# Kernel tuning notes

Hardware: AMD Instinct MI355X
Metric: run time of the kernel (lower is better)

## Reference

```python
import jax, jax.numpy as jnp
import numpy as np

B, S, D = 2, 4096, 768
H, DH = 12, 64
BLK = 64
NB = S // BLK
L, F = 2, 3072
V, POS = 50358, 4096
NS, NL = 8, 2
NKV = 8  # 3 sliding-window + 2 global + 3 random key blocks per query block
SCALE = 1.0 / np.sqrt(DH)


def layer_norm(x, g, b):
    m = jnp.mean(x, -1, keepdims=True)
    v = jnp.mean(jnp.square(x - m), -1, keepdims=True)
    return (x - m) * jax.lax.rsqrt(v + 1e-12) * g + b


def block_sparse_attention(x, mask, w_qkv, b_qkv, rand_blocks):
    # x: [B,S,D], w_qkv: [3,D,D], rand_blocks: [NB,3] int block ids
    qkv = jnp.einsum('bsd,tde->tbse', x, w_qkv) + b_qkv[:, None, None, :]
    q, k, v = [a.reshape(B, S, H, DH).transpose(0, 2, 1, 3) for a in qkv]  # [B,H,S,DH]
    qb = q.reshape(B, H, NB, BLK, DH)
    kb = k.reshape(B, H, NB, BLK, DH)
    vb = v.reshape(B, H, NB, BLK, DH)
    ar = jnp.arange(NB)
    win = jnp.clip(ar[:, None] + jnp.arange(-1, 2)[None, :], 0, NB - 1)  # [NB,3]
    glb = jnp.broadcast_to(jnp.array([0, NB - 1]), (NB, 2))              # [NB,2]
    idx = jnp.concatenate([win, glb, rand_blocks], axis=1)               # [NB,NKV]
    kg = kb[:, :, idx].reshape(B, H, NB, NKV * BLK, DH)                  # gathered keys
    vg = vb[:, :, idx].reshape(B, H, NB, NKV * BLK, DH)
    mg = mask.reshape(B, NB, BLK)[:, idx].reshape(B, NB, NKV * BLK)
    scores = jnp.einsum('bhnqd,bhnkd->bhnqk', qb, kg) * SCALE
    scores = scores + (mg[:, None, :, None, :] - 1.0) * 1e9
    out = jnp.einsum('bhnqk,bhnkd->bhnqd', jax.nn.softmax(scores, -1), vg)  # [B,H,NB,BLK,DH]
    # global query blocks (first/last) attend densely to the full sequence
    qg = jnp.concatenate([qb[:, :, 0], qb[:, :, NB - 1]], axis=2)  # [B,H,2*BLK,DH]
    sg = jnp.einsum('bhqd,bhkd->bhqk', qg, k) * SCALE + (mask[:, None, None, :] - 1.0) * 1e9
    og = jnp.einsum('bhqk,bhkd->bhqd', jax.nn.softmax(sg, -1), v)
    out = out.at[:, :, 0].set(og[:, :, :BLK]).at[:, :, NB - 1].set(og[:, :, BLK:])
    return out.reshape(B, H, S, DH).transpose(0, 2, 1, 3).reshape(B, S, D)


def setup_inputs() -> dict:
    key = jax.random.key(0)
    ks = iter(jax.random.split(key, 40))
    p = lambda shape: (0.02 * jax.random.normal(next(ks), shape)).astype(jnp.float32)
    inp = {}
    inp['input_ids'] = jax.random.randint(next(ks), (B, S), 0, V, dtype=jnp.int32)
    inp['attention_mask'] = jnp.ones((B, S), jnp.float32)
    inp['token_type_ids'] = jnp.zeros((B, S), jnp.int32)
    st = jax.random.randint(next(ks), (B, NS), 0, S - 65, dtype=jnp.int32)
    ln_ = jax.random.randint(next(ks), (B, NS), 1, 65, dtype=jnp.int32)
    inp['spans'] = jnp.stack([st, st + ln_], axis=-1)  # [B,NS,2], start < end
    inp['rand_blocks'] = jax.random.randint(next(ks), (NB, 3), 0, NB, dtype=jnp.int32)
    inp['word_emb'] = p((V, D))
    inp['pos_emb'] = p((POS, D))
    inp['type_emb'] = p((2, D))
    inp['emb_ln_g'] = jnp.ones((D,), jnp.float32)
    inp['emb_ln_b'] = jnp.zeros((D,), jnp.float32)
    inp['qkv_w'] = p((L, 3, D, D))
    inp['qkv_b'] = jnp.zeros((L, 3, D), jnp.float32)
    inp['attn_out_w'] = p((L, D, D))
    inp['attn_out_b'] = jnp.zeros((L, D), jnp.float32)
    inp['ln1_g'] = jnp.ones((L, D), jnp.float32)
    inp['ln1_b'] = jnp.zeros((L, D), jnp.float32)
    inp['ff1_w'] = p((L, D, F))
    inp['ff1_b'] = jnp.zeros((L, F), jnp.float32)
    inp['ff2_w'] = p((L, F, D))
    inp['ff2_b'] = jnp.zeros((L, D), jnp.float32)
    inp['ln2_g'] = jnp.ones((L, D), jnp.float32)
    inp['ln2_b'] = jnp.zeros((L, D), jnp.float32)
    inp['head_w'] = p((D, NL))
    inp['head_b'] = jnp.zeros((NL,), jnp.float32)
    return inp


def reference(input_ids, attention_mask, token_type_ids, spans, rand_blocks,
              word_emb, pos_emb, type_emb, emb_ln_g, emb_ln_b,
              qkv_w, qkv_b, attn_out_w, attn_out_b, ln1_g, ln1_b,
              ff1_w, ff1_b, ff2_w, ff2_b, ln2_g, ln2_b, head_w, head_b):
    h = word_emb[input_ids] + pos_emb[None, :S] + type_emb[token_type_ids]
    h = layer_norm(h, emb_ln_g, emb_ln_b)
    for l in range(L):
        a = block_sparse_attention(h, attention_mask, qkv_w[l], qkv_b[l], rand_blocks)
        h = layer_norm(h + a @ attn_out_w[l] + attn_out_b[l], ln1_g[l], ln1_b[l])
        ff = jax.nn.gelu(h @ ff1_w[l] + ff1_b[l]) @ ff2_w[l] + ff2_b[l]
        h = layer_norm(h + ff, ln2_g[l], ln2_b[l])
    # span mean pooling: mean of h[b, s:e] for each (s,e) span
    starts, ends = spans[..., 0], spans[..., 1]
    pos = jnp.arange(S)
    span_mask = ((pos >= starts[..., None]) & (pos < ends[..., None])).astype(h.dtype)  # [B,NS,S]
    ent = jnp.einsum('bns,bsd->bnd', span_mask, h) / (ends - starts)[..., None].astype(h.dtype)
    pred = ent @ head_w + head_b  # [B,NS,NL]
    return pred.reshape(B * NS, NL)
```

## Files before the change

### kernel.cpp

```cpp
#include <hip/hip_runtime.h>

constexpr int B = 2, S = 4096, D = 768, H = 12, DH = 64, BLK = 64, NB = 64, NKV = 8;
constexpr int F = 3072, NS = 8, M = B * S;
constexpr int NCH = 8;
constexpr float SCALE = 0.125f;
constexpr float L2E = 1.44269504088896f;
constexpr long HD = (long)M * D;

using u16 = unsigned short;
using u32 = unsigned int;
using bf16 = __bf16;
using bf16x8 = __attribute__((ext_vector_type(8))) bf16;
using f32x4 = __attribute__((ext_vector_type(4))) float;

constexpr long DD = (long)D * D;
constexpr long DF = (long)D * F;
constexpr long OFF_AO  = 6 * DD;
constexpr long OFF_FF1 = 8 * DD;
constexpr long OFF_FF2 = 8 * DD + 2 * DF;

__device__ __forceinline__ u16 f2bf(float x) {
  u32 u = __builtin_bit_cast(u32, x);
  u = (u + 0x7fffu + ((u >> 16) & 1u)) >> 16;
  return (u16)u;
}
__device__ __forceinline__ u32 pack2(float a, float b) {
  return (u32)f2bf(a) | ((u32)f2bf(b) << 16);
}
__device__ __forceinline__ float bf2f(u16 v) {
  return __builtin_bit_cast(float, (u32)v << 16);
}
__device__ __forceinline__ float fast_gelu(float x) {
  float u = 0.7978845608028654f * (x + 0.044715f * x * x * x);
  float t = __expf(u + u);
  return x - x * __builtin_amdgcn_rcpf(t + 1.f);
}

__device__ __forceinline__ void gload16(const void* g, void* l) {
  __builtin_amdgcn_global_load_lds(
      (const __attribute__((address_space(1))) u32*)g,
      (__attribute__((address_space(3))) u32*)l, 16, 0, 0);
}

__global__ __launch_bounds__(256) void wtrans_kern(
    const float* __restrict__ in, u16* __restrict__ out, int K, int N, long inz, long outz)
{
  in += (long)blockIdx.z * inz; out += (long)blockIdx.z * outz;
  __shared__ float T[32][33];
  const int n0 = blockIdx.x * 32, k0 = blockIdx.y * 32;
  const int c = threadIdx.x & 31, r8 = threadIdx.x >> 5;
  #pragma unroll
  for (int i = 0; i < 4; ++i)
    T[r8 + i * 8][c] = in[(long)(k0 + r8 + i * 8) * N + n0 + c];
  __syncthreads();
  #pragma unroll
  for (int i = 0; i < 4; ++i)
    out[(long)(n0 + r8 + i * 8) * K + k0 + c] = f2bf(T[c][r8 + i * 8]);
}

__global__ __launch_bounds__(256) void embed_ln_kern(
    const int* __restrict__ ids, const int* __restrict__ tt,
    const float* __restrict__ we, const float* __restrict__ pe, const float* __restrict__ te,
    const float* __restrict__ g, const float* __restrict__ bb,
    u16* __restrict__ h)
{
  const long i = (long)blockIdx.x * 4 + (threadIdx.x >> 6);
  const int lane = threadIdx.x & 63;
  const int c = lane * 4;
  const int s = (int)(i & (S - 1));
  const long wo = (long)ids[i] * D;
  const long to = (long)tt[i] * D;
  const long po = (long)s * D;
  float4 x0, x1, x2;
  {
    float4 a0 = *(const float4*)(we + wo + c),       p0 = *(const float4*)(pe + po + c),
           t0 = *(const float4*)(te + to + c);
    float4 a1 = *(const float4*)(we + wo + c + 256), p1 = *(const float4*)(pe + po + c + 256),
           t1 = *(const float4*)(te + to + c + 256);
    float4 a2 = *(const float4*)(we + wo + c + 512), p2 = *(const float4*)(pe + po + c + 512),
           t2 = *(const float4*)(te + to + c + 512);
    x0 = make_float4(a0.x+p0.x+t0.x, a0.y+p0.y+t0.y, a0.z+p0.z+t0.z, a0.w+p0.w+t0.w);
    x1 = make_float4(a1.x+p1.x+t1.x, a1.y+p1.y+t1.y, a1.z+p1.z+t1.z, a1.w+p1.w+t1.w);
    x2 = make_float4(a2.x+p2.x+t2.x, a2.y+p2.y+t2.y, a2.z+p2.z+t2.z, a2.w+p2.w+t2.w);
  }
  float sm = x0.x+x0.y+x0.z+x0.w + x1.x+x1.y+x1.z+x1.w + x2.x+x2.y+x2.z+x2.w;
  float sq = x0.x*x0.x+x0.y*x0.y+x0.z*x0.z+x0.w*x0.w
           + x1.x*x1.x+x1.y*x1.y+x1.z*x1.z+x1.w*x1.w
           + x2.x*x2.x+x2.y*x2.y+x2.z*x2.z+x2.w*x2.w;
  #pragma unroll
  for (int o = 32; o; o >>= 1) { sm += __shfl_xor(sm, o); sq += __shfl_xor(sq, o); }
  const float mean = sm * (1.f / D);
  const float var  = sq * (1.f / D) - mean * mean;
  const float rs   = rsqrtf(var + 1e-12f);
  float4 g0 = *(const float4*)(g + c),  g1 = *(const float4*)(g + c + 256),
         g2 = *(const float4*)(g + c + 512);
  float4 b0 = *(const float4*)(bb + c), b1 = *(const float4*)(bb + c + 256),
         b2 = *(const float4*)(bb + c + 512);
  u16* rb = h + i * D;
  *(uint2*)(rb + c)       = make_uint2(pack2((x0.x-mean)*rs*g0.x+b0.x, (x0.y-mean)*rs*g0.y+b0.y),
                                       pack2((x0.z-mean)*rs*g0.z+b0.z, (x0.w-mean)*rs*g0.w+b0.w));
  *(uint2*)(rb + c + 256) = make_uint2(pack2((x1.x-mean)*rs*g1.x+b1.x, (x1.y-mean)*rs*g1.y+b1.y),
                                       pack2((x1.z-mean)*rs*g1.z+b1.z, (x1.w-mean)*rs*g1.w+b1.w));
  *(uint2*)(rb + c + 512) = make_uint2(pack2((x2.x-mean)*rs*g2.x+b2.x, (x2.y-mean)*rs*g2.y+b2.y),
                                       pack2((x2.z-mean)*rs*g2.z+b2.z, (x2.w-mean)*rs*g2.w+b2.w));
}

__global__ __launch_bounds__(256) void ln_kern(
    u16* __restrict__ h, const float* __restrict__ g, const float* __restrict__ bb)
{
  const long i = (long)blockIdx.x * 4 + (threadIdx.x >> 6);
  const int lane = threadIdx.x & 63;
  const int c = lane * 4;
  u16* row = h + i * D;
  uint2 u0 = *(const uint2*)(row + c);
  uint2 u1 = *(const uint2*)(row + c + 256);
  uint2 u2 = *(const uint2*)(row + c + 512);
  float x[12];
  x[0] = bf2f(u0.x); x[1] = bf2f(u0.x >> 16); x[2] = bf2f(u0.y); x[3] = bf2f(u0.y >> 16);
  x[4] = bf2f(u1.x); x[5] = bf2f(u1.x >> 16); x[6] = bf2f(u1.y); x[7] = bf2f(u1.y >> 16);
  x[8] = bf2f(u2.x); x[9] = bf2f(u2.x >> 16); x[10] = bf2f(u2.y); x[11] = bf2f(u2.y >> 16);
  float sm = 0.f, sq = 0.f;
  #pragma unroll
  for (int j = 0; j < 12; ++j) { sm += x[j]; sq += x[j] * x[j]; }
  #pragma unroll
  for (int o = 32; o; o >>= 1) { sm += __shfl_xor(sm, o); sq += __shfl_xor(sq, o); }
  const float mean = sm * (1.f / D);
  const float var  = sq * (1.f / D) - mean * mean;
  const float rs   = rsqrtf(var + 1e-12f);
  float4 g0 = *(const float4*)(g + c),  g1 = *(const float4*)(g + c + 256),
         g2 = *(const float4*)(g + c + 512);
  float4 b0 = *(const float4*)(bb + c), b1 = *(const float4*)(bb + c + 256),
         b2 = *(const float4*)(bb + c + 512);
  *(uint2*)(row + c)       = make_uint2(pack2((x[0]-mean)*rs*g0.x+b0.x, (x[1]-mean)*rs*g0.y+b0.y),
                                        pack2((x[2]-mean)*rs*g0.z+b0.z, (x[3]-mean)*rs*g0.w+b0.w));
  *(uint2*)(row + c + 256) = make_uint2(pack2((x[4]-mean)*rs*g1.x+b1.x, (x[5]-mean)*rs*g1.y+b1.y),
                                        pack2((x[6]-mean)*rs*g1.z+b1.z, (x[7]-mean)*rs*g1.w+b1.w));
  *(uint2*)(row + c + 512) = make_uint2(pack2((x[8]-mean)*rs*g2.x+b2.x, (x[9]-mean)*rs*g2.y+b2.y),
                                        pack2((x[10]-mean)*rs*g2.z+b2.z, (x[11]-mean)*rs*g2.w+b2.w));
}

__global__ __launch_bounds__(256) void mgemm_kern(
    const u16* __restrict__ A, const u16* __restrict__ Wt,
    const float* __restrict__ bias, void* __restrict__ Cv,
    int N, int K, long wz, long bz, long cz, int mode, int ksplit)
{
  const int z = blockIdx.z;
  int k0 = 0, kend = K;
  if (ksplit > 1) {
    const int kch = K / ksplit;
    k0 = z * kch; kend = k0 + kch;
  } else {
    Wt += (long)z * wz; bias += (long)z * bz;
  }
  const int gx = gridDim.x;
  const int nwg = gx * gridDim.y;
  int bid = blockIdx.y * gx + blockIdx.x;
  bid = (bid & 7) * (nwg >> 3) + (bid >> 3);
  const long bm = (long)(bid / gx) * 128;
  const int bn = (bid % gx) * 128;

  const int tid = threadIdx.x;
  const int lane = tid & 63, w = tid >> 6;
  const int wm = w >> 1, wn = w & 1;
  const int ls = lane >> 4, lr = lane & 15;

  __shared__ u16 LB[32768];
  u16* const St0 = LB;
  u16* const St1 = LB + 16384;
  float* const LBf = (float*)LB;

  f32x4 acc[4][4];
  #pragma unroll
  for (int i = 0; i < 4; ++i)
    #pragma unroll
    for (int j = 0; j < 4; ++j)
      acc[i][j] = (f32x4){0.f, 0.f, 0.f, 0.f};

  auto STAGE = [&](u16* buf, int kk) {
    #pragma unroll
    for (int c = 0; c < 4; ++c) {
      const int n = (w * 4 + c) * 64 + lane;
      const int row = n >> 3;
      const int kc2 = (n & 7) ^ (row & 7);
      gload16(A  + (bm + row) * K + kk + kc2 * 8, buf + (w * 4 + c) * 512);
      gload16(Wt + (long)(bn + row) * K + kk + kc2 * 8, buf + 8192 + (w * 4 + c) * 512);
    }
  };

  STAGE(St0, k0);
  int cur = 0;
  for (int kk = k0; kk < kend; kk += 64) {
    if (kk + 64 < kend) {
      STAGE(cur ? St0 : St1, kk + 64);
      asm volatile("s_waitcnt vmcnt(8)" ::: "memory");
    } else {
      asm volatile("s_waitcnt vmcnt(0)" ::: "memory");
    }
    __builtin_amdgcn_s_barrier();
    __builtin_amdgcn_sched_barrier(0);
    const u16* AsL = cur ? St1 : St0;
    const u16* BsL = AsL + 8192;
    __builtin_amdgcn_s_setprio(1);
    #pragma unroll
    for (int ks = 0; ks < 2; ++ks) {
      bf16x8 af[4], bv[4];
      const int kc = ks * 4 + ls;
      const int sw = (kc ^ (lr & 7)) << 3;
      #pragma unroll
      for (int mf = 0; mf < 4; ++mf)
        af[mf] = *(const bf16x8*)&AsL[(wm * 64 + mf * 16 + lr) * 64 + sw];
      #pragma unroll
      for (int nf = 0; nf < 4; ++nf)
        bv[nf] = *(const bf16x8*)&BsL[(wn * 64 + nf * 16 + lr) * 64 + sw];
      #pragma unroll
      for (int mf = 0; mf < 4; ++mf)
        #pragma unroll
        for (int nf = 0; nf < 4; ++nf)
          acc[mf][nf] = __builtin_amdgcn_mfma_f32_16x16x32_bf16(
              af[mf], bv[nf], acc[mf][nf], 0, 0, 0);
    }
    __builtin_amdgcn_s_setprio(0);
    __builtin_amdgcn_s_barrier();
    cur ^= 1;
  }

  u16* Cu = (u16*)Cv + (long)z * cz;
  const int r0 = ls * 4;

  if (mode == 2) {
    #pragma unroll
    for (int nf = 0; nf < 4; ++nf) {
      const int col = wn * 64 + nf * 16 + lr;
      const float bvv = bias[bn + col];
      #pragma unroll
      for (int mf = 0; mf < 4; ++mf) {
        #pragma unroll
        for (int r = 0; r < 4; ++r) {
          const int rowl = wm * 64 + mf * 16 + r0 + r;
          LBf[rowl * 128 + (col ^ ((rowl & 7) << 3))] = acc[mf][nf][r] + bvv;
        }
      }
    }
    __syncthreads();
    const int c0 = (tid & 15) * 8;
    #pragma unroll
    for (int i = 0; i < 8; ++i) {
      const int gr = (tid >> 4) + i * 16;
      const int cs = c0 ^ ((gr & 7) << 3);
      float4 a4 = *(const float4*)&LBf[gr * 128 + cs];
      float4 b4 = *(const float4*)&LBf[gr * 128 + cs + 4];
      u16* dst = Cu + (bm + gr) * N + bn + c0;
      uint4 res = *(const uint4*)dst;
      uint4 out;
      out.x = pack2(a4.x + bf2f(res.x), a4.y + bf2f(res.x >> 16));
      out.y = pack2(a4.z + bf2f(res.y), a4.w + bf2f(res.y >> 16));
      out.z = pack2(b4.x + bf2f(res.z), b4.y + bf2f(res.z >> 16));
      out.w = pack2(b4.z + bf2f(res.w), b4.w + bf2f(res.w >> 16));
      *(uint4*)dst = out;
    }
    return;
  }

  if (mode == 1 || (mode == 4 && bn < 1536)) {
    const int t = (mode == 4) ? (bn / 768) : 0;
    const int cl0 = (mode == 4) ? (bn - t * 768) : bn;
    const int Nt = (mode == 4) ? 768 : N;
    u16* Cd = (mode == 4) ? (Cu + (long)t * HD) : Cu;
    #pragma unroll
    for (int nf = 0; nf < 4; ++nf) {
      const int col = wn * 64 + nf * 16 + lr;
      const float bvv = bias[bn + col];
      #pragma unroll
      for (int mf = 0; mf < 4; ++mf) {
        #pragma unroll
        for (int r = 0; r < 4; ++r) {
          const int rowl = wm * 64 + mf * 16 + r0 + r;
          float vv = acc[mf][nf][r] + bvv;
          if (mode == 1) vv = fast_gelu(vv);
          LB[rowl * 128 + (col ^ ((rowl & 7) << 3))] = f2bf(vv);
        }
      }
    }
    __syncthreads();
    const int c0 = (tid & 15) * 8;
    #pragma unroll
    for (int i = 0; i < 8; ++i) {
      const int gr = (tid >> 4) + i * 16;
      uint4 v4 = *(const uint4*)&LB[gr * 128 + (c0 ^ ((gr & 7) << 3))];
      *(uint4*)(Cd + (bm + gr) * Nt + cl0 + c0) = v4;
    }
    return;
  }

  #pragma unroll
  for (int nf = 0; nf < 4; ++nf) {
    const int cl = bn - 1536 + wn * 64 + nf * 16 + lr;
    const int hcol = cl >> 6, dcol = cl & 63;
    const float bvv = bias[1536 + cl];
    #pragma unroll
    for (int mf = 0; mf < 4; ++mf) {
      const long t0 = bm + wm * 64 + mf * 16 + r0;
      const int bb2 = (int)(t0 >> 12), s0 = (int)(t0 & (S - 1));
      const float v0 = acc[mf][nf][0] + bvv, v1 = acc[mf][nf][1] + bvv;
      const float v2 = acc[mf][nf][2] + bvv, v3 = acc[mf][nf][3] + bvv;
      *(uint2*)(Cu + 2 * HD + (((long)bb2 * H + hcol) * 64 + dcol) * S + s0) =
          make_uint2(pack2(v0, v1), pack2(v2, v3));
    }
  }
}

__global__ __launch_bounds__(256) void mattn_kern(
    const u16* __restrict__ q, const u16* __restrict__ k, const u16* __restrict__ vt,
    const float* __restrict__ mask, const int* __restrict__ rb,
    u16* __restrict__ ctx, float* __restrict__ part)
{
  int lin = blockIdx.x;
  lin = (lin & 7) * 234 + (lin >> 3);
  const int x  = lin % 78;
  const int hh = (lin / 78) % H;
  const int b  = lin / 936;

  int qb, kv0, nkv, qb2 = 0, ch = 0, dense;
  if (x < 62) { dense = 0; qb = x + 1; kv0 = 0; nkv = NKV; }
  else {
    dense = 1;
    const int dx = x - 62;
    qb2 = dx >> 3; ch = dx & 7;
    qb = qb2 ? NB - 1 : 0; kv0 = ch * (NB / NCH); nkv = NB / NCH;
  }
  const int tid = threadIdx.x, lane = tid & 63, w = tid >> 6;
  const int lr = lane & 15, hi = lane >> 4;

  __shared__ u16 KV[2][8192];
  __shared__ u16 Ps[64][72];

  const long qrow0 = (long)b * S + qb * 64;
  bf16x8 qf[2];
  {
    const u16* qp = q + (qrow0 + w * 16 + lr) * D + hh * 64 + hi * 8;
    qf[0] = *(const bf16x8*)(qp);
    qf[1] = *(const bf16x8*)(qp + 32);
  }
  const long vtbase = (((long)b * H + hh) * 64) * S;

  bf16x8 ones8;
  #pragma unroll
  for (int i = 0; i < 8; ++i) ones8[i] = __builtin_bit_cast(bf16, (u16)0x3F80);

  auto kbof = [&](int j) -> int {
    if (dense) return kv0 + j;
    if (j < 3) return qb - 1 + j;
    if (j == 3) return 0;
    if (j == 4) return NB - 1;
    return rb[qb * 3 + (j - 5)];
  };

  auto STAGE = [&](u16* st, int kb) {
    const long krow0 = (long)b * S + kb * 64;
    #pragma unroll
    for (int c = 0; c < 2; ++c) {
      const int n = (w * 2 + c) * 64 + lane;
      const int row = n >> 3;
      const int g2 = (n & 7) ^ (row & 7);
      gload16(k + (krow0 + row) * D + hh * 64 + g2 * 8, st + (w * 2 + c) * 512);
      gload16(vt + vtbase + (long)row * S + kb * 64 + g2 * 8, st + 4096 + (w * 2 + c) * 512);
    }
  };

  f32x4 acc[4];
  #pragma unroll
  for (int nf = 0; nf < 4; ++nf) acc[nf] = (f32x4){0.f, 0.f, 0.f, 0.f};
  f32x4 lacc = (f32x4){0.f, 0.f, 0.f, 0.f};
  float m_run = -1e30f;

  const float C2 = SCALE * L2E;

  float4 mk4[4];
  auto LOADMASK = [&](int kb) {
    const long r = (long)b * S + kb * 64;
    #pragma unroll
    for (int kf = 0; kf < 4; ++kf)
      mk4[kf] = *(const float4*)(mask + r + kf * 16 + hi * 4);
  };

  STAGE(KV[0], kbof(0));
  LOADMASK(kbof(0));

  for (int jj = 0; jj < nkv; ++jj) {
    if (jj + 1 < nkv) {
      STAGE(KV[(jj + 1) & 1], kbof(jj + 1));
      asm volatile("s_waitcnt vmcnt(4)" ::: "memory");
    } else {
      asm volatile("s_waitcnt vmcnt(0)" ::: "memory");
    }
    __builtin_amdgcn_s_barrier();
    __builtin_amdgcn_sched_barrier(0);

    const u16* Ks = KV[jj & 1];
    const u16* Vs = Ks + 4096;

    f32x4 sc[4];
    #pragma unroll
    for (int kf = 0; kf < 4; ++kf) sc[kf] = (f32x4){0.f, 0.f, 0.f, 0.f};
    __builtin_amdgcn_s_setprio(1);
    #pragma unroll
    for (int kc = 0; kc < 2; ++kc) {
      #pragma unroll
      for (int kf = 0; kf < 4; ++kf) {
        const int g2 = ((kc * 4 + hi) ^ (lr & 7)) << 3;
        bf16x8 kfr = *(const bf16x8*)&Ks[(kf * 16 + lr) * 64 + g2];
        sc[kf] = __builtin_amdgcn_mfma_f32_16x16x32_bf16(kfr, qf[kc], sc[kf], 0, 0, 0);
      }
    }
    __builtin_amdgcn_s_setprio(0);

    float sv[4][4];
    float mx = -3.0e38f;
    #pragma unroll
    for (int kf = 0; kf < 4; ++kf) {
      const float mka[4] = {mk4[kf].x, mk4[kf].y, mk4[kf].z, mk4[kf].w};
      #pragma unroll
      for (int r = 0; r < 4; ++r) {
        sv[kf][r] = sc[kf][r] * C2 + (mka[r] - 1.f) * (1e9f * L2E);
        mx = fmaxf(mx, sv[kf][r]);
      }
    }
    mx = fmaxf(mx, __shfl_xor(mx, 16));
    mx = fmaxf(mx, __shfl_xor(mx, 32));
    const bool need = mx > m_run + 8.f;
    if (__any((int)need)) {
      const float mn = fmaxf(m_run, mx);
      const float al = exp2f(m_run - mn);
      m_run = mn;
      #pragma unroll
      for (int r = 0; r < 4; ++r) {
        const float alr = __shfl(al, (lane & 48) | (hi * 4 + r));
        lacc[r] *= alr;
        acc[0][r] *= alr; acc[1][r] *= alr; acc[2][r] *= alr; acc[3][r] *= alr;
      }
    }
    {
      const int prow = w * 16 + lr;
      #pragma unroll
      for (int kf = 0; kf < 4; ++kf) {
        u32 lo = pack2(exp2f(sv[kf][0] - m_run), exp2f(sv[kf][1] - m_run));
        u32 hi2 = pack2(exp2f(sv[kf][2] - m_run), exp2f(sv[kf][3] - m_run));
        *(uint2*)&Ps[prow][kf * 16 + hi * 4] = make_uint2(lo, hi2);
      }
    }

    __builtin_amdgcn_s_setprio(1);
    #pragma unroll
    for (int kc = 0; kc < 2; ++kc) {
      bf16x8 pf = *(const bf16x8*)&Ps[w * 16 + lr][kc * 32 + hi * 8];
      #pragma unroll
      for (int nf = 0; nf < 4; ++nf) {
        const int g2 = ((kc * 4 + hi) ^ (lr & 7)) << 3;
        bf16x8 vfr = *(const bf16x8*)&Vs[(nf * 16 + lr) * 64 + g2];
        acc[nf] = __builtin_amdgcn_mfma_f32_16x16x32_bf16(pf, vfr, acc[nf], 0, 0, 0);
      }
      lacc = __builtin_amdgcn_mfma_f32_16x16x32_bf16(pf, ones8, lacc, 0, 0, 0);
    }
    __builtin_amdgcn_s_setprio(0);

    if (jj + 1 < nkv) LOADMASK(kbof(jj + 1));

    __builtin_amdgcn_s_barrier();
  }

  if (!dense) {
    #pragma unroll
    for (int r = 0; r < 4; ++r) {
      const float inv = 1.f / lacc[r];
      const int prow = w * 16 + hi * 4 + r;
      Ps[prow][ 0 + lr] = f2bf(acc[0][r] * inv);
      Ps[prow][16 + lr] = f2bf(acc[1][r] * inv);
      Ps[prow][32 + lr] = f2bf(acc[2][r] * inv);
      Ps[prow][48 + lr] = f2bf(acc[3][r] * inv);
    }
    __syncthreads();
    const int r2 = tid >> 2, c2 = (tid & 3) * 16;
    uint4 v0 = *(const uint4*)&Ps[r2][c2];
    uint4 v1 = *(const uint4*)&Ps[r2][c2 + 8];
    u16* op = ctx + (qrow0 + r2) * D + hh * 64 + c2;
    *(uint4*)(op)     = v0;
    *(uint4*)(op + 8) = v1;
  } else {
    const long pb = ((((long)b * H + hh) * 2 + qb2) * NCH + ch) * (64 * 68);
    #pragma unroll
    for (int r = 0; r < 4; ++r) {
      const float m_r = __shfl(m_run, (lane & 48) | (hi * 4 + r));
      float* pp = part + pb + (w * 16 + hi * 4 + r) * 68;
      pp[ 0 + lr] = acc[0][r];
      pp[16 + lr] = acc[1][r];
      pp[32 + lr] = acc[2][r];
      pp[48 + lr] = acc[3][r];
      if (lr == 0) { pp[64] = m_r; pp[65] = lacc[r]; }
    }
  }
}

__global__ __launch_bounds__(256) void attn_combine_kern(
    const float* __restrict__ part, u16* __restrict__ ctx)
{
  const int g = blockIdx.x;
  const int qb2 = g & 1;
  const int hh = (g >> 1) % H;
  const int b  = g / (2 * H);
  const int r  = threadIdx.x >> 2;
  const int d0 = (threadIdx.x & 3) * 16;
  const long pb = (long)g * NCH * 64 * 68;
  float mg = -1e30f;
  for (int ch = 0; ch < NCH; ++ch)
    mg = fmaxf(mg, part[pb + ch * 64 * 68 + r * 68 + 64]);
  float lg = 0.f;
  float a[16] = {};
  for (int ch = 0; ch < NCH; ++ch) {
    const float* pp = part + pb + ch * 64 * 68 + r * 68;
    const float w = exp2f(pp[64] - mg);
    lg += pp[65] * w;
    #pragma unroll
    for (int i = 0; i < 4; ++i) {
      float4 t4 = *(const float4*)(pp + d0 + i * 4);
      a[i*4+0] += t4.x * w; a[i*4+1] += t4.y * w; a[i*4+2] += t4.z * w; a[i*4+3] += t4.w * w;
    }
  }
  const int qb = qb2 ? NB - 1 : 0;
  const float inv = 1.f / lg;
  u16* op = ctx + ((long)b * S + qb * 64 + r) * D + hh * 64 + d0;
  #pragma unroll
  for (int i = 0; i < 4; ++i)
    *(uint2*)(op + i * 4) = make_uint2(pack2(a[i*4+0]*inv, a[i*4+1]*inv),
                                       pack2(a[i*4+2]*inv, a[i*4+3]*inv));
}

__global__ __launch_bounds__(256) void span_head_kern(
    const u16* __restrict__ h, const int* __restrict__ spans,
    const float* __restrict__ hw, const float* __restrict__ hb, float* __restrict__ out)
{
  __shared__ float s0[4], s1[4];
  const int bn = blockIdx.x;
  const int tid = threadIdx.x;
  const int st = spans[bn * 2], en = spans[bn * 2 + 1];
  const int b = bn >> 3;
  float a0 = 0.f, a1 = 0.f, a2 = 0.f;
  for (int s = st; s < en; ++s) {
    const u16* row = h + ((long)b * S + s) * D;
    a0 += bf2f(row[tid]); a1 += bf2f(row[tid + 256]); a2 += bf2f(row[tid + 512]);
  }
  const float inv = 1.f / (float)(en - st);
  a0 *= inv; a1 *= inv; a2 *= inv;
  float p0 = a0 * hw[tid * 2]     + a1 * hw[(tid + 256) * 2]     + a2 * hw[(tid + 512) * 2];
  float p1 = a0 * hw[tid * 2 + 1] + a1 * hw[(tid + 256) * 2 + 1] + a2 * hw[(tid + 512) * 2 + 1];
  #pragma unroll
  for (int o = 32; o; o >>= 1) { p0 += __shfl_xor(p0, o); p1 += __shfl_xor(p1, o); }
  if ((tid & 63) == 0) { s0[tid >> 6] = p0; s1[tid >> 6] = p1; }
  __syncthreads();
  if (tid == 0) {
    out[bn * 2]     = s0[0] + s0[1] + s0[2] + s0[3] + hb[0];
    out[bn * 2 + 1] = s1[0] + s1[1] + s1[2] + s1[3] + hb[1];
  }
}

extern "C" void kernel_launch(void* const* d_in, const int* in_sizes, int n_in,
                              void* d_out, int out_size, void* d_ws, size_t ws_size,
                              hipStream_t stream) {
  const int*   input_ids  = (const int*)  d_in[0];
  const float* attn_mask  = (const float*)d_in[1];
  const int*   tok_type   = (const int*)  d_in[2];
  const int*   spans      = (const int*)  d_in[3];
  const int*   rand_blk   = (const int*)  d_in[4];
  const float* word_emb   = (const float*)d_in[5];
  const float* pos_emb    = (const float*)d_in[6];
  const float* type_emb   = (const float*)d_in[7];
  const float* emb_g      = (const float*)d_in[8];
  const float* emb_b      = (const float*)d_in[9];
  const float* qkv_w      = (const float*)d_in[10];
  const float* qkv_b      = (const float*)d_in[11];
  const float* aow        = (const float*)d_in[12];
  const float* aob        = (const float*)d_in[13];
  const float* ln1g       = (const float*)d_in[14];
  const float* ln1b       = (const float*)d_in[15];
  const float* ff1w       = (const float*)d_in[16];
  const float* ff1b       = (const float*)d_in[17];
  const float* ff2w       = (const float*)d_in[18];
  const float* ff2b       = (const float*)d_in[19];
  const float* ln2g       = (const float*)d_in[20];
  const float* ln2b       = (const float*)d_in[21];
  const float* headw      = (const float*)d_in[22];
  const float* headb      = (const float*)d_in[23];

  float* ws    = (float*)d_ws;
  u16*   h     = (u16*)ws;
  u16*   qkvb  = (u16*)(ws + HD);
  u16*   ffb   = (u16*)(ws + HD);
  u16*   ctx16 = (u16*)(ws + 3 * HD);
  float* part  = ws + 4 * HD;
  u16*   wb    = (u16*)(ws + 4 * HD + HD/2);

  wtrans_kern<<<dim3(24, 24, 6), dim3(256), 0, stream>>>(qkv_w, wb, D, D, DD, DD);
  wtrans_kern<<<dim3(24, 24, 2), dim3(256), 0, stream>>>(aow, wb + OFF_AO, D, D, DD, DD);
  wtrans_kern<<<dim3(96, 24, 2), dim3(256), 0, stream>>>(ff1w, wb + OFF_FF1, D, F, DF, DF);
  wtrans_kern<<<dim3(24, 96, 2), dim3(256), 0, stream>>>(ff2w, wb + OFF_FF2, F, D, DF, DF);

  embed_ln_kern<<<dim3(M / 4), dim3(256), 0, stream>>>(
      input_ids, tok_type, word_emb, pos_emb, type_emb, emb_g, emb_b, h);

  for (int l = 0; l < 2; ++l) {
    mgemm_kern<<<dim3(18, 64, 1), dim3(256), 0, stream>>>(
        h, wb + (long)l * 3 * DD, qkv_b + (long)l * 3 * D, qkvb, 2304, D, 0, 0, 0, 4, 1);
    mattn_kern<<<dim3(1872), dim3(256), 0, stream>>>(
        qkvb, qkvb + HD, qkvb + 2 * HD, attn_mask, rand_blk, ctx16, part);
    attn_combine_kern<<<dim3(B * H * 2), dim3(256), 0, stream>>>(part, ctx16);
    mgemm_kern<<<dim3(6, 64, 1), dim3(256), 0, stream>>>(
        ctx16, wb + OFF_AO + (long)l * DD, aob + (long)l * D, h, D, D, 0, 0, 0, 2, 1);
    ln_kern<<<dim3(M / 4), dim3(256), 0, stream>>>(h, ln1g + (long)l * D, ln1b + (long)l * D);
    mgemm_kern<<<dim3(24, 64, 1), dim3(256), 0, stream>>>(
        h, wb + OFF_FF1 + (long)l * DF, ff1b + (long)l * F, ffb, F, D, 0, 0, 0, 1, 1);
    mgemm_kern<<<dim3(6, 64, 1), dim3(256), 0, stream>>>(
        ffb, wb + OFF_FF2 + (long)l * DF, ff2b + (long)l * D, h, D, F, 0, 0, 0, 2, 1);
    ln_kern<<<dim3(M / 4), dim3(256), 0, stream>>>(h, ln2g + (long)l * D, ln2b + (long)l * D);
  }

  span_head_kern<<<dim3(B * NS), dim3(256), 0, stream>>>(h, spans, headw, headb, (float*)d_out);
}
```

Before: 547.2 us.

## Single-buffer A tile in GEMM to cut LDS footprint and raise occupancy

Only the weight (B) tile stays double-buffered. The activation (A) tile becomes a single LDS buffer that is reloaded after the compute barrier, which shrinks shared memory from 64KB to 48KB per workgroup. The mode-2 residual epilogue now stages the fp32 output in two 64-row halves so it fits in the smaller buffer. The aim is more resident workgroups per CU. The cost is that A loads are no longer overlapped with compute, since they are issued only after the barrier and waited on before the next iteration.

Result: slower. 586.3 us (+7.1%).

```diff
diff --git a/kernel.cpp b/kernel.cpp
--- a/kernel.cpp
+++ b/kernel.cpp
@@ -164,10 +164,10 @@
   const int wm = w >> 1, wn = w & 1;
   const int ls = lane >> 4, lr = lane & 15;
 
-  __shared__ u16 LB[32768];
-  u16* const St0 = LB;
-  u16* const St1 = LB + 16384;
-  float* const LBf = (float*)LB;
+  __shared__ u16 LB[24576];
+  u16* const As = LB;
+  u16* const B0 = LB + 8192;
+  u16* const B1 = LB + 16384;
 
   f32x4 acc[4][4];
   #pragma unroll
@@ -176,30 +176,39 @@
     for (int j = 0; j < 4; ++j)
       acc[i][j] = (f32x4){0.f, 0.f, 0.f, 0.f};
 
-  auto STAGE = [&](u16* buf, int kk) {
+  auto STAGE_A = [&](int kk) {
     #pragma unroll
     for (int c = 0; c < 4; ++c) {
       const int n = (w * 4 + c) * 64 + lane;
       const int row = n >> 3;
       const int kc2 = (n & 7) ^ (row & 7);
-      gload16(A  + (bm + row) * K + kk + kc2 * 8, buf + (w * 4 + c) * 512);
-      gload16(Wt + (long)(bn + row) * K + kk + kc2 * 8, buf + 8192 + (w * 4 + c) * 512);
+      gload16(A + (bm + row) * K + kk + kc2 * 8, As + (w * 4 + c) * 512);
     }
   };
-
-  STAGE(St0, k0);
+  auto STAGE_B = [&](u16* buf, int kk) {
+    #pragma unroll
+    for (int c = 0; c < 4; ++c) {
+      const int n = (w * 4 + c) * 64 + lane;
+      const int row = n >> 3;
+      const int kc2 = (n & 7) ^ (row & 7);
+      gload16(Wt + (long)(bn + row) * K + kk + kc2 * 8, buf + (w * 4 + c) * 512);
+    }
+  };
+
+  STAGE_B(B0, k0);
+  STAGE_A(k0);
   int cur = 0;
   for (int kk = k0; kk < kend; kk += 64) {
-    if (kk + 64 < kend) {
-      STAGE(cur ? St0 : St1, kk + 64);
-      asm volatile("s_waitcnt vmcnt(8)" ::: "memory");
+    const bool hasNext = (kk + 64 < kend);
+    if (hasNext) {
+      STAGE_B(cur ? B0 : B1, kk + 64);
+      asm volatile("s_waitcnt vmcnt(4)" ::: "memory");
     } else {
       asm volatile("s_waitcnt vmcnt(0)" ::: "memory");
     }
     __builtin_amdgcn_s_barrier();
     __builtin_amdgcn_sched_barrier(0);
-    const u16* AsL = cur ? St1 : St0;
-    const u16* BsL = AsL + 8192;
+    const u16* BsL = cur ? B1 : B0;
     __builtin_amdgcn_s_setprio(1);
     #pragma unroll
     for (int ks = 0; ks < 2; ++ks) {
@@ -208,7 +217,7 @@
       const int sw = (kc ^ (lr & 7)) << 3;
       #pragma unroll
       for (int mf = 0; mf < 4; ++mf)
-        af[mf] = *(const bf16x8*)&AsL[(wm * 64 + mf * 16 + lr) * 64 + sw];
+        af[mf] = *(const bf16x8*)&As[(wm * 64 + mf * 16 + lr) * 64 + sw];
       #pragma unroll
       for (int nf = 0; nf < 4; ++nf)
         bv[nf] = *(const bf16x8*)&BsL[(wn * 64 + nf * 16 + lr) * 64 + sw];
@@ -221,6 +230,7 @@
     }
     __builtin_amdgcn_s_setprio(0);
     __builtin_amdgcn_s_barrier();
+    if (hasNext) STAGE_A(kk + 64);
     cur ^= 1;
   }
 
@@ -228,35 +238,42 @@
   const int r0 = ls * 4;
 
   if (mode == 2) {
-    #pragma unroll
-    for (int nf = 0; nf < 4; ++nf) {
-      const int col = wn * 64 + nf * 16 + lr;
-      const float bvv = bias[bn + col];
-      #pragma unroll
-      for (int mf = 0; mf < 4; ++mf) {
+    float* const LBf = (float*)LB;
+    #pragma unroll
+    for (int half = 0; half < 2; ++half) {
+      if (wm == half) {
         #pragma unroll
-        for (int r = 0; r < 4; ++r) {
-          const int rowl = wm * 64 + mf * 16 + r0 + r;
-          LBf[rowl * 128 + (col ^ ((rowl & 7) << 3))] = acc[mf][nf][r] + bvv;
+        for (int nf = 0; nf < 4; ++nf) {
+          const int col = wn * 64 + nf * 16 + lr;
+          const float bvv = bias[bn + col];
+          #pragma unroll
+          for (int mf = 0; mf < 4; ++mf) {
+            #pragma unroll
+            for (int r = 0; r < 4; ++r) {
+              const int rl = mf * 16 + r0 + r;
+              LBf[rl * 128 + (col ^ ((rl & 7) << 3))] = acc[mf][nf][r] + bvv;
+            }
+          }
         }
       }
-    }
-    __syncthreads();
-    const int c0 = (tid & 15) * 8;
-    #pragma unroll
-    for (int i = 0; i < 8; ++i) {
-      const int gr = (tid >> 4) + i * 16;
-      const int cs = c0 ^ ((gr & 7) << 3);
-      float4 a4 = *(const float4*)&LBf[gr * 128 + cs];
-      float4 b4 = *(const float4*)&LBf[gr * 128 + cs + 4];
-      u16* dst = Cu + (bm + gr) * N + bn + c0;
-      uint4 res = *(const uint4*)dst;
-      uint4 out;
-      out.x = pack2(a4.x + bf2f(res.x), a4.y + bf2f(res.x >> 16));
-      out.y = pack2(a4.z + bf2f(res.y), a4.w + bf2f(res.y >> 16));
-      out.z = pack2(b4.x + bf2f(res.z), b4.y + bf2f(res.z >> 16));
-      out.w = pack2(b4.z + bf2f(res.w), b4.w + bf2f(res.w >> 16));
-      *(uint4*)dst = out;
+      __syncthreads();
+      const int c0 = (tid & 15) * 8;
+      #pragma unroll
+      for (int i = 0; i < 4; ++i) {
+        const int grl = (tid >> 4) + i * 16;
+        const int cs = c0 ^ ((grl & 7) << 3);
+        float4 a4 = *(const float4*)&LBf[grl * 128 + cs];
+        float4 b4 = *(const float4*)&LBf[grl * 128 + cs + 4];
+        u16* dst = Cu + (bm + half * 64 + grl) * N + bn + c0;
+        uint4 res = *(const uint4*)dst;
+        uint4 out;
+        out.x = pack2(a4.x + bf2f(res.x), a4.y + bf2f(res.x >> 16));
+        out.y = pack2(a4.z + bf2f(res.y), a4.w + bf2f(res.y >> 16));
+        out.z = pack2(b4.x + bf2f(res.z), b4.y + bf2f(res.z >> 16));
+        out.w = pack2(b4.z + bf2f(res.w), b4.w + bf2f(res.w >> 16));
+        *(uint4*)dst = out;
+      }
+      __syncthreads();
     }
     return;
   }
```
